# Kernel optimization log

Measured on AMD Instinct MI355X. Metric: run time of the kernel, lower is better.

## Reference

```python
import jax, jax.numpy as jnp
import numpy as np

D_MODEL = 512
NUM_HEADS = 8
D_K = D_MODEL // NUM_HEADS
SCALE = 1.0 / np.sqrt(D_K).astype(np.float32)


def _relative_shift(x):
    # x: (B, H, S, P) pos scores from Q @ P^T; Transformer-XL shift trick.
    b, h, s, p = x.shape
    x = jnp.pad(x, ((0, 0), (0, 0), (0, 0), (1, 0)))   # (B,H,S,P+1)
    x = x.reshape(b, h, p + 1, s)[:, :, 1:, :]          # drop first row
    x = x.reshape(b, h, s, p)[:, :, :, :s]
    return x


def setup_inputs() -> dict:
    key = jax.random.key(0)
    ks = jax.random.split(key, 10)
    B, S = 4, 2048
    glorot = lambda k: jax.random.uniform(
        k, (D_MODEL, D_MODEL), jnp.float32,
        -np.sqrt(6.0 / (2 * D_MODEL)), np.sqrt(6.0 / (2 * D_MODEL)))
    return {
        "inputs": jax.random.normal(ks[0], (B, S, D_MODEL), jnp.float32),
        "pos_enc": jax.random.normal(ks[1], (1, S, D_MODEL), jnp.float32),
        "W_q": glorot(ks[2]),
        "W_k": glorot(ks[3]),
        "W_v": glorot(ks[4]),
        "W_o": glorot(ks[5]),
        "W_pos": glorot(ks[6]),
        "u_bias": jnp.zeros((NUM_HEADS, D_K), jnp.float32),
        "v_bias": jnp.zeros((NUM_HEADS, D_K), jnp.float32),
    }


def reference(inputs, pos_enc, W_q, W_k, W_v, W_o, W_pos, u_bias, v_bias):
    B, S, _ = inputs.shape
    split = lambda x, b: x.reshape(b, S, NUM_HEADS, D_K).transpose(0, 2, 1, 3)
    Q = split(inputs @ W_q, B)        # (B,H,S,dk)
    K = split(inputs @ W_k, B)
    V = split(inputs @ W_v, B)
    P = split(pos_enc @ W_pos, 1)      # (1,H,S,dk)
    u = u_bias[None, :, None, :]
    v = v_bias[None, :, None, :]
    content_score = jnp.einsum('bhid,bhjd->bhij', Q + u, K)
    pos_score = jnp.einsum('bhid,xhjd->bhij', Q + v, P)  # broadcast over batch
    pos_score = _relative_shift(pos_score)
    scores = (content_score + pos_score) * SCALE
    attn = jax.nn.softmax(scores, axis=-1)  # no dropout (inference)
    context = jnp.einsum('bhij,bhjd->bhid', attn, V)
    context = context.transpose(0, 2, 1, 3).reshape(B, S, D_MODEL)
    return context @ W_o
```

## Files before the change

kernel.cpp:

```cpp
#include <hip/hip_runtime.h>
#include <hip/hip_bf16.h>
#include <math.h>

#define SEQ 2048
#define NH 8
#define DK 64
#define DM 512
#define QSCALE 0.18033688011112042f
#define PPAD (SEQ + 128)
#define POFF 64
#define KSTR 72
#define PSTR 36
#define ASTR 34

typedef unsigned short ushortT;
typedef short s16x8 __attribute__((ext_vector_type(8)));
typedef float f32x4 __attribute__((ext_vector_type(4)));

#define MFMA16 __builtin_amdgcn_mfma_f32_16x16x32_bf16

static __device__ __forceinline__ ushortT f2bf(float x) {
  __hip_bfloat16 h = __float2bfloat16(x);
  ushortT u;
  __builtin_memcpy(&u, &h, 2);
  return u;
}

static __device__ __forceinline__ float fexp2(float x) {
  return __builtin_amdgcn_exp2f(x);
}

static __device__ __forceinline__ s16x8 pack8(const float* p) {
  ushortT u[8];
#pragma unroll
  for (int i = 0; i < 8; ++i) u[i] = f2bf(p[i]);
  s16x8 out;
  __builtin_memcpy(&out, u, 16);
  return out;
}

static __device__ __forceinline__ int pinv(int j) {
  return (j < 16) ? ((j >> 2) * 8 + (j & 3)) : (((j >> 2) - 4) * 8 + 4 + (j & 3));
}

__global__ __launch_bounds__(256)
void cast_in(const float* __restrict__ X, const float* __restrict__ PE,
             ushortT* __restrict__ Xb, ushortT* __restrict__ PEb) {
  const size_t i4 = (size_t)blockIdx.x * 256 + threadIdx.x;
  const size_t NX = (size_t)4 * SEQ * DM / 4;
  const float4 v = (i4 < NX) ? *(const float4*)(X + i4 * 4)
                             : *(const float4*)(PE + (i4 - NX) * 4);
  ushortT o[4] = {f2bf(v.x), f2bf(v.y), f2bf(v.z), f2bf(v.w)};
  ushortT* dst = (i4 < NX) ? (Xb + i4 * 4) : (PEb + (i4 - NX) * 4);
  *(ulonglong1*)dst = *(ulonglong1*)o;
}

__global__ __launch_bounds__(256)
void transpose_w(const float* __restrict__ w0, const float* __restrict__ w1,
                 const float* __restrict__ w2, const float* __restrict__ w3,
                 const float* __restrict__ w4, ushortT* __restrict__ out) {
  __shared__ float ts[32][33];
  const int z = blockIdx.z;
  const float* w = (z == 0) ? w0 : (z == 1) ? w1 : (z == 2) ? w2 : (z == 3) ? w3 : w4;
  ushortT* o = out + (size_t)z * DM * DM;
  const int k0 = blockIdx.x * 32, n0 = blockIdx.y * 32;
  const int tx = threadIdx.x, ty = threadIdx.y;
#pragma unroll
  for (int i = 0; i < 4; ++i)
    ts[ty + i * 8][tx] = w[(size_t)(k0 + ty + i * 8) * DM + n0 + tx];
  __syncthreads();
#pragma unroll
  for (int i = 0; i < 4; ++i)
    o[(size_t)(n0 + ty + i * 8) * DM + k0 + tx] = f2bf(ts[tx][ty + i * 8]);
}

__global__ __launch_bounds__(256)
void gemm_mfma(const ushortT* __restrict__ A, const ushortT* __restrict__ Bt,
               const float* __restrict__ ubv, const float* __restrict__ vbv,
               ushortT* __restrict__ qu, ushortT* __restrict__ qv,
               ushortT* __restrict__ kb, ushortT* __restrict__ vt,
               float* __restrict__ of, int mode) {
  __shared__ ushortT As[128][ASTR];
  __shared__ ushortT Bs[128][ASTR];
  const int tid = threadIdx.x;
  const int w = tid >> 6, lane = tid & 63;
  const int c = lane & 15, q = lane >> 4;
  const int wm = w >> 1, wn = w & 1;
  const int m0 = blockIdx.x * 128, n0 = blockIdx.y * 128;
  const int lr = tid >> 1, lh = (tid & 1) * 16;

  f32x4 acc[4][4];
#pragma unroll
  for (int mt = 0; mt < 4; ++mt)
#pragma unroll
    for (int nt = 0; nt < 4; ++nt) acc[mt][nt] = (f32x4){0.f, 0.f, 0.f, 0.f};

  const ushortT* Ar = A + (size_t)(m0 + lr) * DM + lh;
  const ushortT* Br = Bt + (size_t)(n0 + lr) * DM + lh;
  uint4 a0 = *(const uint4*)(Ar);
  uint4 a1 = *(const uint4*)(Ar + 8);
  uint4 b0 = *(const uint4*)(Br);
  uint4 b1 = *(const uint4*)(Br + 8);

  for (int k0 = 0; k0 < DM; k0 += 32) {
    __syncthreads();
    *(uint4*)&As[lr][lh] = a0; *(uint4*)&As[lr][lh + 8] = a1;
    *(uint4*)&Bs[lr][lh] = b0; *(uint4*)&Bs[lr][lh + 8] = b1;
    __syncthreads();
    if (k0 + 32 < DM) {
      a0 = *(const uint4*)(Ar + k0 + 32);
      a1 = *(const uint4*)(Ar + k0 + 40);
      b0 = *(const uint4*)(Br + k0 + 32);
      b1 = *(const uint4*)(Br + k0 + 40);
    }
    s16x8 af[4], bf[4];
#pragma unroll
    for (int mt = 0; mt < 4; ++mt)
      af[mt] = *(const s16x8*)&As[wm * 64 + mt * 16 + c][q * 8];
#pragma unroll
    for (int nt = 0; nt < 4; ++nt)
      bf[nt] = *(const s16x8*)&Bs[wn * 64 + nt * 16 + c][q * 8];
#pragma unroll
    for (int mt = 0; mt < 4; ++mt)
#pragma unroll
      for (int nt = 0; nt < 4; ++nt)
        acc[mt][nt] = MFMA16(af[mt], bf[nt], acc[mt][nt], 0, 0, 0);
  }

#pragma unroll
  for (int mt = 0; mt < 4; ++mt)
#pragma unroll
    for (int nt = 0; nt < 4; ++nt)
#pragma unroll
      for (int r = 0; r < 4; ++r) {
        const int gm = m0 + wm * 64 + mt * 16 + q * 4 + r;
        const int gn = n0 + wn * 64 + nt * 16 + c;
        const float v = acc[mt][nt][r];
        const int bb = gm >> 11, s = gm & (SEQ - 1);
        if (mode == 0) {
          const int z = gn >> 9, gn5 = gn & 511;
          const int h = gn5 >> 6, d = gn5 & 63;
          if (z == 0) {
            const size_t base = (((size_t)bb * NH + h) * SEQ + s) * DK + d;
            qu[base] = f2bf((v + ubv[gn5]) * QSCALE);
            qv[base] = f2bf((v + vbv[gn5]) * QSCALE);
          } else if (z == 1) {
            kb[(((size_t)bb * NH + h) * SEQ + s) * DK + d] = f2bf(v);
          } else {
            const int s_il = (s & ~31) | pinv(s & 31);
            vt[(((size_t)bb * NH + h) * DK + d) * SEQ + s_il] = f2bf(v);
          }
        } else if (mode == 3) {
          const int h = gn >> 6, d = gn & 63;
          qu[((size_t)h * PPAD + POFF + gm) * DK + d] = f2bf(v);
        } else {
          of[(size_t)gm * DM + gn] = v;
        }
      }
}

static __device__ __forceinline__ f32x4 band_gemm(const ushortT* pb, int tile,
                                                  int c, int q, s16x8 a0, s16x8 a1) {
  const ushortT* pc = pb + (ptrdiff_t)(tile * 16 + c) * DK + q * 8;
  f32x4 G = {0.f, 0.f, 0.f, 0.f};
  G = MFMA16(a0, *(const s16x8*)pc, G, 0, 0, 0);
  G = MFMA16(a1, *(const s16x8*)(pc + 32), G, 0, 0, 0);
  return G;
}

__global__ __launch_bounds__(256, 3)
void attn_mfma(const ushortT* __restrict__ Qu, const ushortT* __restrict__ Qv,
               const ushortT* __restrict__ Kb, const ushortT* __restrict__ Vt,
               const ushortT* __restrict__ Pp, ushortT* __restrict__ ctxb) {
  const int n = blockIdx.x;
  const int xcd = n & 7, idx = n >> 3;
  const int b = idx >> 5, iblk = idx & 31;
  const int h = xcd, bh = b * 8 + h;
  const int tid = threadIdx.x;
  const int w = tid >> 6, lane = tid & 63;
  const int c = lane & 15, q = lane >> 4;
  const int i0 = iblk * 64;
  const int iw = i0 + w * 16;

  __shared__ ushortT Ks[64][KSTR];
  __shared__ ushortT Vs[64][KSTR];
  __shared__ float E1[4][16][PSTR];
  __shared__ float E2[4][16][PSTR];
  __shared__ float Lb[4][16];

  const ushortT* Qub = Qu + ((size_t)bh * SEQ + iw) * DK;
  const ushortT* Qvb = Qv + ((size_t)bh * SEQ + iw) * DK;
  const ushortT* Kbh = Kb + (size_t)bh * SEQ * DK;
  const ushortT* Vbh = Vt + (size_t)bh * DK * SEQ;
  const ushortT* Ph  = Pp + ((size_t)h * PPAD + POFF) * DK;

  const s16x8 qu0 = *(const s16x8*)(Qub + (size_t)c * DK + q * 8);
  const s16x8 qu1 = *(const s16x8*)(Qub + (size_t)c * DK + 32 + q * 8);
  s16x8 qv0 = *(const s16x8*)(Qvb + (size_t)c * DK + q * 8);
  s16x8 qv1 = *(const s16x8*)(Qvb + (size_t)c * DK + 32 + q * 8);

  int joff[8];
#pragma unroll
  for (int jj = 0; jj < 8; ++jj)
    joff[jj] = (jj < 4) ? (4 * q + jj) : (16 + 4 * q + (jj - 4));

  f32x4 O[4];
#pragma unroll
  for (int r = 0; r < 4; ++r) O[r] = (f32x4){0.f, 0.f, 0.f, 0.f};
  float lrow = 0.f;
  f32x4 e[3];
  bool hv1 = false, hv2 = false;
  const int jt = iw & ~31;
  const int m_w = q * 4;

  {
    const ushortT* gk = Kbh;
    uint4 k0v = *(const uint4*)(gk + tid * 8);
    uint4 k1v = *(const uint4*)(gk + 2048 + tid * 8);
    const ushortT* gv = Vbh + (size_t)(tid >> 2) * SEQ + (tid & 3) * 16;
    uint4 v0v = *(const uint4*)gv;
    uint4 v1v = *(const uint4*)(gv + 8);
    *(uint4*)&Ks[tid >> 3][(tid & 7) * 8] = k0v;
    *(uint4*)&Ks[32 + (tid >> 3)][(tid & 7) * 8] = k1v;
    *(uint4*)&Vs[tid >> 2][(tid & 3) * 16] = v0v;
    *(uint4*)&Vs[tid >> 2][(tid & 3) * 16 + 8] = v1v;
  }
  __syncthreads();

#define WRITE_BAND(ARR, ev)                                                   \
  _Pragma("unroll")                                                           \
  for (int t = 0; t < 3; ++t)                                                 \
    _Pragma("unroll")                                                         \
    for (int r = 0; r < 4; ++r) {                                             \
      const int kcol = t * 16 + c + (m_w + r) - 15;                           \
      if (kcol >= 0 && kcol < 32) ARR[w][m_w + r][pinv(kcol)] = (ev)[t][r];   \
    }

#define PV_FROM(pr, jl)                                                       \
  {                                                                           \
    lrow += pr[0] + pr[1] + pr[2] + pr[3] + pr[4] + pr[5] + pr[6] + pr[7];    \
    const s16x8 pa = pack8(pr);                                               \
    _Pragma("unroll")                                                         \
    for (int dt = 0; dt < 4; ++dt) {                                          \
      const s16x8 vb = *(const s16x8*)&Vs[dt * 16 + c][(jl) + q * 8];         \
      O[dt] = MFMA16(pa, vb, O[dt], 0, 0, 0);                                 \
    }                                                                         \
  }

  for (int ch = 0; ch < 32; ++ch) {
    const bool more = (ch + 1) < 32;
    uint4 k0v, k1v, v0v, v1v;
    if (more) {
      const ushortT* gk = Kbh + (size_t)(ch + 1) * 64 * DK;
      k0v = *(const uint4*)(gk + tid * 8);
      k1v = *(const uint4*)(gk + 2048 + tid * 8);
      const ushortT* gv = Vbh + (size_t)(tid >> 2) * SEQ + (ch + 1) * 64 + (tid & 3) * 16;
      v0v = *(const uint4*)gv;
      v1v = *(const uint4*)(gv + 8);
    }
#pragma unroll
    for (int t = 0; t < 2; ++t) {
      const int j0 = ch * 64 + t * 32;
      const int jl = t * 32;
      const int drel = j0 - iw;
      f32x4 S0 = {0.f, 0.f, 0.f, 0.f}, S1 = {0.f, 0.f, 0.f, 0.f};
      {
        const ushortT* ka = &Ks[jl + c][q * 8];
        S0 = MFMA16(*(const s16x8*)ka, qu0, S0, 0, 0, 0);
        S0 = MFMA16(*(const s16x8*)(ka + 32), qu1, S0, 0, 0, 0);
        const ushortT* ka2 = &Ks[jl + 16 + c][q * 8];
        S1 = MFMA16(*(const s16x8*)ka2, qu0, S1, 0, 0, 0);
        S1 = MFMA16(*(const s16x8*)(ka2 + 32), qu1, S1, 0, 0, 0);
      }
      if (j0 < jt) {
        const ushortT* pb1 = Ph + (ptrdiff_t)(drel + SEQ - 16) * DK;
        if (hv1) e[0] = e[2];
        else { e[0] = band_gemm(pb1, 0, c, q, qv0, qv1); hv1 = true; }
        e[1] = band_gemm(pb1, 1, c, q, qv0, qv1);
        e[2] = band_gemm(pb1, 2, c, q, qv0, qv1);
        WRITE_BAND(E1, e)
        const float* e1r = &E1[w][c][q * 8];
        float4 fA = *(const float4*)e1r, fB = *(const float4*)(e1r + 4);
        float pr[8] = {fexp2(S0[0] + fA.x), fexp2(S0[1] + fA.y),
                       fexp2(S0[2] + fA.z), fexp2(S0[3] + fA.w),
                       fexp2(S1[0] + fB.x), fexp2(S1[1] + fB.y),
                       fexp2(S1[2] + fB.z), fexp2(S1[3] + fB.w)};
        PV_FROM(pr, jl)
      } else if (j0 < jt + 64) {
        {
          const ushortT* pb1 = Ph + (ptrdiff_t)(drel + SEQ - 16) * DK;
          f32x4 t1[3];
          t1[0] = band_gemm(pb1, 0, c, q, qv0, qv1);
          t1[1] = band_gemm(pb1, 1, c, q, qv0, qv1);
          t1[2] = band_gemm(pb1, 2, c, q, qv0, qv1);
          WRITE_BAND(E1, t1)
        }
        {
          const s16x8 qw0 = *(const s16x8*)(Qvb + (size_t)(c + 1) * DK + q * 8);
          const s16x8 qw1 = *(const s16x8*)(Qvb + (size_t)(c + 1) * DK + 32 + q * 8);
          const ushortT* pb2 = Ph + (ptrdiff_t)(drel - 17) * DK;
          f32x4 t2[3];
          t2[0] = band_gemm(pb2, 0, c, q, qw0, qw1);
          t2[1] = band_gemm(pb2, 1, c, q, qw0, qw1);
          t2[2] = band_gemm(pb2, 2, c, q, qw0, qw1);
          WRITE_BAND(E2, t2)
        }
        const float* e1r = &E1[w][c][q * 8];
        const float* e2r = &E2[w][c][q * 8];
        float4 aA = *(const float4*)e1r, aB = *(const float4*)(e1r + 4);
        float4 bA = *(const float4*)e2r, bB = *(const float4*)(e2r + 4);
        float f1[8] = {aA.x, aA.y, aA.z, aA.w, aB.x, aB.y, aB.z, aB.w};
        float f2[8] = {bA.x, bA.y, bA.z, bA.w, bB.x, bB.y, bB.z, bB.w};
        float sv[8] = {S0[0], S0[1], S0[2], S0[3], S1[0], S1[1], S1[2], S1[3]};
        float pr[8];
#pragma unroll
        for (int jj = 0; jj < 8; ++jj) {
          const int dlt = drel + joff[jj] - c;
          const float g = (dlt <= 0) ? f1[jj] : ((dlt == 1) ? 0.0f : f2[jj]);
          pr[jj] = fexp2(sv[jj] + g);
        }
        PV_FROM(pr, jl)
      } else {
        if (!hv2) {
          qv0 = *(const s16x8*)(Qvb + (size_t)(c + 1) * DK + q * 8);
          qv1 = *(const s16x8*)(Qvb + (size_t)(c + 1) * DK + 32 + q * 8);
        }
        const ushortT* pb2 = Ph + (ptrdiff_t)(drel - 17) * DK;
        if (hv2) e[0] = e[2];
        else { e[0] = band_gemm(pb2, 0, c, q, qv0, qv1); hv2 = true; }
        e[1] = band_gemm(pb2, 1, c, q, qv0, qv1);
        e[2] = band_gemm(pb2, 2, c, q, qv0, qv1);
        WRITE_BAND(E1, e)
        const float* e1r = &E1[w][c][q * 8];
        float4 fA = *(const float4*)e1r, fB = *(const float4*)(e1r + 4);
        float pr[8] = {fexp2(S0[0] + fA.x), fexp2(S0[1] + fA.y),
                       fexp2(S0[2] + fA.z), fexp2(S0[3] + fA.w),
                       fexp2(S1[0] + fB.x), fexp2(S1[1] + fB.y),
                       fexp2(S1[2] + fB.z), fexp2(S1[3] + fB.w)};
        PV_FROM(pr, jl)
      }
    }
    __syncthreads();
    if (more) {
      *(uint4*)&Ks[tid >> 3][(tid & 7) * 8] = k0v;
      *(uint4*)&Ks[32 + (tid >> 3)][(tid & 7) * 8] = k1v;
      *(uint4*)&Vs[tid >> 2][(tid & 3) * 16] = v0v;
      *(uint4*)&Vs[tid >> 2][(tid & 3) * 16 + 8] = v1v;
    }
    __syncthreads();
  }

  lrow += __shfl_xor(lrow, 16);
  lrow += __shfl_xor(lrow, 32);
  if (q == 0) Lb[w][c] = lrow;
  float inv[4];
#pragma unroll
  for (int r = 0; r < 4; ++r) inv[r] = 1.0f / Lb[w][q * 4 + r];
#pragma unroll
  for (int dt = 0; dt < 4; ++dt)
#pragma unroll
    for (int r = 0; r < 4; ++r) {
      const int i = iw + q * 4 + r;
      ctxb[((size_t)b * SEQ + i) * DM + h * DK + dt * 16 + c] = f2bf(O[dt][r] * inv[r]);
    }
}

extern "C" void kernel_launch(void* const* d_in, const int* in_sizes, int n_in,
                              void* d_out, int out_size, void* d_ws, size_t ws_size,
                              hipStream_t stream) {
  (void)in_sizes; (void)n_in; (void)out_size; (void)ws_size;
  const float* X   = (const float*)d_in[0];
  const float* PE  = (const float*)d_in[1];
  const float* Wq  = (const float*)d_in[2];
  const float* Wk  = (const float*)d_in[3];
  const float* Wv  = (const float*)d_in[4];
  const float* Wo  = (const float*)d_in[5];
  const float* Wp  = (const float*)d_in[6];
  const float* ubv = (const float*)d_in[7];
  const float* vbv = (const float*)d_in[8];

  const size_t NX = (size_t)4 * SEQ * DM;
  const size_t NP = (size_t)SEQ * DM;
  const size_t NW = (size_t)DM * DM;
  ushortT* Xb  = (ushortT*)d_ws;
  ushortT* PEb = Xb + NX;
  ushortT* Wt  = PEb + NP;
  ushortT* qu  = Wt + 5 * NW;
  ushortT* qv  = qu + NX;
  ushortT* kb  = qv + NX;
  ushortT* vt  = kb + NX;
  ushortT* pp  = vt + NX;
  ushortT* ctx = pp + (size_t)NH * PPAD * DK;
  float* outp = (float*)d_out;

  hipLaunchKernelGGL(cast_in, dim3((NX + NP) / 4 / 256), dim3(256), 0, stream, X, PE, Xb, PEb);
  hipLaunchKernelGGL(transpose_w, dim3(16, 16, 5), dim3(32, 8), 0, stream, Wq, Wk, Wv, Wp, Wo, Wt);
  dim3 blk(256);
  hipLaunchKernelGGL(gemm_mfma, dim3(64, 12), blk, 0, stream, Xb, Wt, ubv, vbv,
                     qu, qv, kb, vt, (float*)nullptr, 0);
  hipLaunchKernelGGL(gemm_mfma, dim3(16, 4), blk, 0, stream, PEb, Wt + 3 * NW, ubv, vbv,
                     pp, (ushortT*)nullptr, (ushortT*)nullptr, (ushortT*)nullptr, (float*)nullptr, 3);
  hipLaunchKernelGGL(attn_mfma, dim3(1024), blk, 0, stream, qu, qv, kb, vt, pp, ctx);
  hipLaunchKernelGGL(gemm_mfma, dim3(64, 4), blk, 0, stream, ctx, Wt + 4 * NW, ubv, vbv,
                     (ushortT*)nullptr, (ushortT*)nullptr, (ushortT*)nullptr, (ushortT*)nullptr, outp, 4);
}
```

Measured before the change: 375.1 us.

## Use single-wave attention blocks loading K/V fragments directly from global memory

The attention kernel moves from 256-thread blocks that stage 64-key K/V chunks in shared memory, with two barriers per chunk, to 64-thread single-wave blocks (4096 of them). Each wave loads its K and V MFMA fragments straight from global memory for each 32-key step. The row-sum normalization now uses a wave shuffle instead of shared memory. This removes the barriers and the LDS staging, but K/V reuse across the four waves is lost, so global/L2 traffic rises about fourfold and load latency is no longer hidden by prefetching.

```diff
diff --git a/kernel.cpp b/kernel.cpp
--- a/kernel.cpp
+++ b/kernel.cpp
@@ -9,7 +9,6 @@
 #define QSCALE 0.18033688011112042f
 #define PPAD (SEQ + 128)
 #define POFF 64
-#define KSTR 72
 #define PSTR 36
 #define ASTR 34
 
@@ -168,25 +167,20 @@
   return G;
 }
 
-__global__ __launch_bounds__(256, 3)
+__global__ __launch_bounds__(64, 4)
 void attn_mfma(const ushortT* __restrict__ Qu, const ushortT* __restrict__ Qv,
                const ushortT* __restrict__ Kb, const ushortT* __restrict__ Vt,
                const ushortT* __restrict__ Pp, ushortT* __restrict__ ctxb) {
   const int n = blockIdx.x;
-  const int xcd = n & 7, idx = n >> 3;
-  const int b = idx >> 5, iblk = idx & 31;
-  const int h = xcd, bh = b * 8 + h;
-  const int tid = threadIdx.x;
-  const int w = tid >> 6, lane = tid & 63;
+  const int h = n & 7, idx = n >> 3;
+  const int b = idx >> 7;
+  const int iw = (idx & 127) * 16;
+  const int bh = b * 8 + h;
+  const int lane = threadIdx.x;
   const int c = lane & 15, q = lane >> 4;
-  const int i0 = iblk * 64;
-  const int iw = i0 + w * 16;
-
-  __shared__ ushortT Ks[64][KSTR];
-  __shared__ ushortT Vs[64][KSTR];
-  __shared__ float E1[4][16][PSTR];
-  __shared__ float E2[4][16][PSTR];
-  __shared__ float Lb[4][16];
+
+  __shared__ float E1[16][PSTR];
+  __shared__ float E2[16][PSTR];
 
   const ushortT* Qub = Qu + ((size_t)bh * SEQ + iw) * DK;
   const ushortT* Qvb = Qv + ((size_t)bh * SEQ + iw) * DK;
@@ -213,149 +207,117 @@
   const int jt = iw & ~31;
   const int m_w = q * 4;
 
-  {
-    const ushortT* gk = Kbh;
-    uint4 k0v = *(const uint4*)(gk + tid * 8);
-    uint4 k1v = *(const uint4*)(gk + 2048 + tid * 8);
-    const ushortT* gv = Vbh + (size_t)(tid >> 2) * SEQ + (tid & 3) * 16;
-    uint4 v0v = *(const uint4*)gv;
-    uint4 v1v = *(const uint4*)(gv + 8);
-    *(uint4*)&Ks[tid >> 3][(tid & 7) * 8] = k0v;
-    *(uint4*)&Ks[32 + (tid >> 3)][(tid & 7) * 8] = k1v;
-    *(uint4*)&Vs[tid >> 2][(tid & 3) * 16] = v0v;
-    *(uint4*)&Vs[tid >> 2][(tid & 3) * 16 + 8] = v1v;
-  }
-  __syncthreads();
-
 #define WRITE_BAND(ARR, ev)                                                   \
   _Pragma("unroll")                                                           \
   for (int t = 0; t < 3; ++t)                                                 \
     _Pragma("unroll")                                                         \
     for (int r = 0; r < 4; ++r) {                                             \
       const int kcol = t * 16 + c + (m_w + r) - 15;                           \
-      if (kcol >= 0 && kcol < 32) ARR[w][m_w + r][pinv(kcol)] = (ev)[t][r];   \
+      if (kcol >= 0 && kcol < 32) ARR[m_w + r][pinv(kcol)] = (ev)[t][r];      \
     }
 
-#define PV_FROM(pr, jl)                                                       \
+#define PV_FROM(pr)                                                           \
   {                                                                           \
     lrow += pr[0] + pr[1] + pr[2] + pr[3] + pr[4] + pr[5] + pr[6] + pr[7];    \
     const s16x8 pa = pack8(pr);                                               \
     _Pragma("unroll")                                                         \
-    for (int dt = 0; dt < 4; ++dt) {                                          \
-      const s16x8 vb = *(const s16x8*)&Vs[dt * 16 + c][(jl) + q * 8];         \
-      O[dt] = MFMA16(pa, vb, O[dt], 0, 0, 0);                                 \
-    }                                                                         \
+    for (int dt = 0; dt < 4; ++dt)                                            \
+      O[dt] = MFMA16(pa, vb[dt], O[dt], 0, 0, 0);                             \
   }
 
-  for (int ch = 0; ch < 32; ++ch) {
-    const bool more = (ch + 1) < 32;
-    uint4 k0v, k1v, v0v, v1v;
-    if (more) {
-      const ushortT* gk = Kbh + (size_t)(ch + 1) * 64 * DK;
-      k0v = *(const uint4*)(gk + tid * 8);
-      k1v = *(const uint4*)(gk + 2048 + tid * 8);
-      const ushortT* gv = Vbh + (size_t)(tid >> 2) * SEQ + (ch + 1) * 64 + (tid & 3) * 16;
-      v0v = *(const uint4*)gv;
-      v1v = *(const uint4*)(gv + 8);
+  for (int jb = 0; jb < 64; ++jb) {
+    const int j0 = jb * 32;
+    const int drel = j0 - iw;
+
+    const s16x8 kf0 = *(const s16x8*)(Kbh + (size_t)(j0 + c) * DK + q * 8);
+    const s16x8 kf1 = *(const s16x8*)(Kbh + (size_t)(j0 + c) * DK + 32 + q * 8);
+    const s16x8 kf2 = *(const s16x8*)(Kbh + (size_t)(j0 + 16 + c) * DK + q * 8);
+    const s16x8 kf3 = *(const s16x8*)(Kbh + (size_t)(j0 + 16 + c) * DK + 32 + q * 8);
+    s16x8 vb[4];
+#pragma unroll
+    for (int dt = 0; dt < 4; ++dt)
+      vb[dt] = *(const s16x8*)(Vbh + (size_t)(dt * 16 + c) * SEQ + j0 + q * 8);
+
+    f32x4 S0 = {0.f, 0.f, 0.f, 0.f}, S1 = {0.f, 0.f, 0.f, 0.f};
+    S0 = MFMA16(kf0, qu0, S0, 0, 0, 0);
+    S0 = MFMA16(kf1, qu1, S0, 0, 0, 0);
+    S1 = MFMA16(kf2, qu0, S1, 0, 0, 0);
+    S1 = MFMA16(kf3, qu1, S1, 0, 0, 0);
+
+    if (j0 < jt) {
+      const ushortT* pb1 = Ph + (ptrdiff_t)(drel + SEQ - 16) * DK;
+      if (hv1) e[0] = e[2];
+      else { e[0] = band_gemm(pb1, 0, c, q, qv0, qv1); hv1 = true; }
+      e[1] = band_gemm(pb1, 1, c, q, qv0, qv1);
+      e[2] = band_gemm(pb1, 2, c, q, qv0, qv1);
+      WRITE_BAND(E1, e)
+      const float* e1r = &E1[c][q * 8];
+      float4 fA = *(const float4*)e1r, fB = *(const float4*)(e1r + 4);
+      float pr[8] = {fexp2(S0[0] + fA.x), fexp2(S0[1] + fA.y),
+                     fexp2(S0[2] + fA.z), fexp2(S0[3] + fA.w),
+                     fexp2(S1[0] + fB.x), fexp2(S1[1] + fB.y),
+                     fexp2(S1[2] + fB.z), fexp2(S1[3] + fB.w)};
+      PV_FROM(pr)
+    } else if (j0 < jt + 64) {
+      {
+        const ushortT* pb1 = Ph + (ptrdiff_t)(drel + SEQ - 16) * DK;
+        f32x4 t1[3];
+        t1[0] = band_gemm(pb1, 0, c, q, qv0, qv1);
+        t1[1] = band_gemm(pb1, 1, c, q, qv0, qv1);
+        t1[2] = band_gemm(pb1, 2, c, q, qv0, qv1);
+        WRITE_BAND(E1, t1)
+      }
+      {
+        const s16x8 qw0 = *(const s16x8*)(Qvb + (size_t)(c + 1) * DK + q * 8);
+        const s16x8 qw1 = *(const s16x8*)(Qvb + (size_t)(c + 1) * DK + 32 + q * 8);
+        const ushortT* pb2 = Ph + (ptrdiff_t)(drel - 17) * DK;
+        f32x4 t2[3];
+        t2[0] = band_gemm(pb2, 0, c, q, qw0, qw1);
+        t2[1] = band_gemm(pb2, 1, c, q, qw0, qw1);
+        t2[2] = band_gemm(pb2, 2, c, q, qw0, qw1);
+        WRITE_BAND(E2, t2)
+      }
+      const float* e1r = &E1[c][q * 8];
+      const float* e2r = &E2[c][q * 8];
+      float4 aA = *(const float4*)e1r, aB = *(const float4*)(e1r + 4);
+      float4 bA = *(const float4*)e2r, bB = *(const float4*)(e2r + 4);
+      float f1[8] = {aA.x, aA.y, aA.z, aA.w, aB.x, aB.y, aB.z, aB.w};
+      float f2[8] = {bA.x, bA.y, bA.z, bA.w, bB.x, bB.y, bB.z, bB.w};
+      float sv[8] = {S0[0], S0[1], S0[2], S0[3], S1[0], S1[1], S1[2], S1[3]};
+      float pr[8];
+#pragma unroll
+      for (int jj = 0; jj < 8; ++jj) {
+        const int dlt = drel + joff[jj] - c;
+        const float g = (dlt <= 0) ? f1[jj] : ((dlt == 1) ? 0.0f : f2[jj]);
+        pr[jj] = fexp2(sv[jj] + g);
+      }
+      PV_FROM(pr)
+    } else {
+      if (!hv2) {
+        qv0 = *(const s16x8*)(Qvb + (size_t)(c + 1) * DK + q * 8);
+        qv1 = *(const s16x8*)(Qvb + (size_t)(c + 1) * DK + 32 + q * 8);
+      }
+      const ushortT* pb2 = Ph + (ptrdiff_t)(drel - 17) * DK;
+      if (hv2) e[0] = e[2];
+      else { e[0] = band_gemm(pb2, 0, c, q, qv0, qv1); hv2 = true; }
+      e[1] = band_gemm(pb2, 1, c, q, qv0, qv1);
+      e[2] = band_gemm(pb2, 2, c, q, qv0, qv1);
+      WRITE_BAND(E1, e)
+      const float* e1r = &E1[c][q * 8];
+      float4 fA = *(const float4*)e1r, fB = *(const float4*)(e1r + 4);
+      float pr[8] = {fexp2(S0[0] + fA.x), fexp2(S0[1] + fA.y),
+                     fexp2(S0[2] + fA.z), fexp2(S0[3] + fA.w),
+                     fexp2(S1[0] + fB.x), fexp2(S1[1] + fB.y),
+                     fexp2(S1[2] + fB.z), fexp2(S1[3] + fB.w)};
+      PV_FROM(pr)
     }
-#pragma unroll
-    for (int t = 0; t < 2; ++t) {
-      const int j0 = ch * 64 + t * 32;
-      const int jl = t * 32;
-      const int drel = j0 - iw;
-      f32x4 S0 = {0.f, 0.f, 0.f, 0.f}, S1 = {0.f, 0.f, 0.f, 0.f};
-      {
-        const ushortT* ka = &Ks[jl + c][q * 8];
-        S0 = MFMA16(*(const s16x8*)ka, qu0, S0, 0, 0, 0);
-        S0 = MFMA16(*(const s16x8*)(ka + 32), qu1, S0, 0, 0, 0);
-        const ushortT* ka2 = &Ks[jl + 16 + c][q * 8];
-        S1 = MFMA16(*(const s16x8*)ka2, qu0, S1, 0, 0, 0);
-        S1 = MFMA16(*(const s16x8*)(ka2 + 32), qu1, S1, 0, 0, 0);
-      }
-      if (j0 < jt) {
-        const ushortT* pb1 = Ph + (ptrdiff_t)(drel + SEQ - 16) * DK;
-        if (hv1) e[0] = e[2];
-        else { e[0] = band_gemm(pb1, 0, c, q, qv0, qv1); hv1 = true; }
-        e[1] = band_gemm(pb1, 1, c, q, qv0, qv1);
-        e[2] = band_gemm(pb1, 2, c, q, qv0, qv1);
-        WRITE_BAND(E1, e)
-        const float* e1r = &E1[w][c][q * 8];
-        float4 fA = *(const float4*)e1r, fB = *(const float4*)(e1r + 4);
-        float pr[8] = {fexp2(S0[0] + fA.x), fexp2(S0[1] + fA.y),
-                       fexp2(S0[2] + fA.z), fexp2(S0[3] + fA.w),
-                       fexp2(S1[0] + fB.x), fexp2(S1[1] + fB.y),
-                       fexp2(S1[2] + fB.z), fexp2(S1[3] + fB.w)};
-        PV_FROM(pr, jl)
-      } else if (j0 < jt + 64) {
-        {
-          const ushortT* pb1 = Ph + (ptrdiff_t)(drel + SEQ - 16) * DK;
-          f32x4 t1[3];
-          t1[0] = band_gemm(pb1, 0, c, q, qv0, qv1);
-          t1[1] = band_gemm(pb1, 1, c, q, qv0, qv1);
-          t1[2] = band_gemm(pb1, 2, c, q, qv0, qv1);
-          WRITE_BAND(E1, t1)
-        }
-        {
-          const s16x8 qw0 = *(const s16x8*)(Qvb + (size_t)(c + 1) * DK + q * 8);
-          const s16x8 qw1 = *(const s16x8*)(Qvb + (size_t)(c + 1) * DK + 32 + q * 8);
-          const ushortT* pb2 = Ph + (ptrdiff_t)(drel - 17) * DK;
-          f32x4 t2[3];
-          t2[0] = band_gemm(pb2, 0, c, q, qw0, qw1);
-          t2[1] = band_gemm(pb2, 1, c, q, qw0, qw1);
-          t2[2] = band_gemm(pb2, 2, c, q, qw0, qw1);
-          WRITE_BAND(E2, t2)
-        }
-        const float* e1r = &E1[w][c][q * 8];
-        const float* e2r = &E2[w][c][q * 8];
-        float4 aA = *(const float4*)e1r, aB = *(const float4*)(e1r + 4);
-        float4 bA = *(const float4*)e2r, bB = *(const float4*)(e2r + 4);
-        float f1[8] = {aA.x, aA.y, aA.z, aA.w, aB.x, aB.y, aB.z, aB.w};
-        float f2[8] = {bA.x, bA.y, bA.z, bA.w, bB.x, bB.y, bB.z, bB.w};
-        float sv[8] = {S0[0], S0[1], S0[2], S0[3], S1[0], S1[1], S1[2], S1[3]};
-        float pr[8];
-#pragma unroll
-        for (int jj = 0; jj < 8; ++jj) {
-          const int dlt = drel + joff[jj] - c;
-          const float g = (dlt <= 0) ? f1[jj] : ((dlt == 1) ? 0.0f : f2[jj]);
-          pr[jj] = fexp2(sv[jj] + g);
-        }
-        PV_FROM(pr, jl)
-      } else {
-        if (!hv2) {
-          qv0 = *(const s16x8*)(Qvb + (size_t)(c + 1) * DK + q * 8);
-          qv1 = *(const s16x8*)(Qvb + (size_t)(c + 1) * DK + 32 + q * 8);
-        }
-        const ushortT* pb2 = Ph + (ptrdiff_t)(drel - 17) * DK;
-        if (hv2) e[0] = e[2];
-        else { e[0] = band_gemm(pb2, 0, c, q, qv0, qv1); hv2 = true; }
-        e[1] = band_gemm(pb2, 1, c, q, qv0, qv1);
-        e[2] = band_gemm(pb2, 2, c, q, qv0, qv1);
-        WRITE_BAND(E1, e)
-        const float* e1r = &E1[w][c][q * 8];
-        float4 fA = *(const float4*)e1r, fB = *(const float4*)(e1r + 4);
-        float pr[8] = {fexp2(S0[0] + fA.x), fexp2(S0[1] + fA.y),
-                       fexp2(S0[2] + fA.z), fexp2(S0[3] + fA.w),
-                       fexp2(S1[0] + fB.x), fexp2(S1[1] + fB.y),
-                       fexp2(S1[2] + fB.z), fexp2(S1[3] + fB.w)};
-        PV_FROM(pr, jl)
-      }
-    }
-    __syncthreads();
-    if (more) {
-      *(uint4*)&Ks[tid >> 3][(tid & 7) * 8] = k0v;
-      *(uint4*)&Ks[32 + (tid >> 3)][(tid & 7) * 8] = k1v;
-      *(uint4*)&Vs[tid >> 2][(tid & 3) * 16] = v0v;
-      *(uint4*)&Vs[tid >> 2][(tid & 3) * 16 + 8] = v1v;
-    }
-    __syncthreads();
   }
 
   lrow += __shfl_xor(lrow, 16);
   lrow += __shfl_xor(lrow, 32);
-  if (q == 0) Lb[w][c] = lrow;
   float inv[4];
 #pragma unroll
-  for (int r = 0; r < 4; ++r) inv[r] = 1.0f / Lb[w][q * 4 + r];
+  for (int r = 0; r < 4; ++r) inv[r] = 1.0f / __shfl(lrow, m_w + r);
 #pragma unroll
   for (int dt = 0; dt < 4; ++dt)
 #pragma unroll
@@ -400,7 +362,7 @@
                      qu, qv, kb, vt, (float*)nullptr, 0);
   hipLaunchKernelGGL(gemm_mfma, dim3(16, 4), blk, 0, stream, PEb, Wt + 3 * NW, ubv, vbv,
                      pp, (ushortT*)nullptr, (ushortT*)nullptr, (ushortT*)nullptr, (float*)nullptr, 3);
-  hipLaunchKernelGGL(attn_mfma, dim3(1024), blk, 0, stream, qu, qv, kb, vt, pp, ctx);
+  hipLaunchKernelGGL(attn_mfma, dim3(4096), dim3(64), 0, stream, qu, qv, kb, vt, pp, ctx);
   hipLaunchKernelGGL(gemm_mfma, dim3(64, 4), blk, 0, stream, ctx, Wt + 4 * NW, ubv, vbv,
                      (ushortT*)nullptr, (ushortT*)nullptr, (ushortT*)nullptr, (ushortT*)nullptr, outp, 4);
 }
```

Measured after the change: 527.9 us. +40.7%, slower.

## Software-pipeline positional band GEMM one tile ahead with double-buffered LDS

Applied to the files above, without the earlier changes.

Computes the relative-position band scores for the next 32-column tile after the current tile's softmax and PV work, storing them in a double-buffered E1 LDS array. The aim is to hide the latency of the band MFMAs, the global P loads and the LDS write/read round trip behind independent work. The shifted Qv rows (qw) are now loaded once up front. This raises LDS use and register pressure, which could lower occupancy at the 3-blocks-per-SM launch bound.

```diff
diff --git a/kernel.cpp b/kernel.cpp
--- a/kernel.cpp
+++ b/kernel.cpp
@@ -168,6 +168,18 @@
   return G;
 }
 
+static __device__ __forceinline__ void write_band(float (*E)[PSTR], int c, int m_w,
+                                                  f32x4 b0, f32x4 b1, f32x4 b2) {
+  const f32x4 bb[3] = {b0, b1, b2};
+#pragma unroll
+  for (int t = 0; t < 3; ++t)
+#pragma unroll
+    for (int r = 0; r < 4; ++r) {
+      const int kcol = t * 16 + c + (m_w + r) - 15;
+      if (kcol >= 0 && kcol < 32) E[m_w + r][pinv(kcol)] = bb[t][r];
+    }
+}
+
 __global__ __launch_bounds__(256, 3)
 void attn_mfma(const ushortT* __restrict__ Qu, const ushortT* __restrict__ Qv,
                const ushortT* __restrict__ Kb, const ushortT* __restrict__ Vt,
@@ -184,7 +196,7 @@
 
   __shared__ ushortT Ks[64][KSTR];
   __shared__ ushortT Vs[64][KSTR];
-  __shared__ float E1[4][16][PSTR];
+  __shared__ float E1[4][2][16][PSTR];
   __shared__ float E2[4][16][PSTR];
   __shared__ float Lb[4][16];
 
@@ -196,8 +208,10 @@
 
   const s16x8 qu0 = *(const s16x8*)(Qub + (size_t)c * DK + q * 8);
   const s16x8 qu1 = *(const s16x8*)(Qub + (size_t)c * DK + 32 + q * 8);
-  s16x8 qv0 = *(const s16x8*)(Qvb + (size_t)c * DK + q * 8);
-  s16x8 qv1 = *(const s16x8*)(Qvb + (size_t)c * DK + 32 + q * 8);
+  const s16x8 qv0 = *(const s16x8*)(Qvb + (size_t)c * DK + q * 8);
+  const s16x8 qv1 = *(const s16x8*)(Qvb + (size_t)c * DK + 32 + q * 8);
+  const s16x8 qw0 = *(const s16x8*)(Qvb + (size_t)(c + 1) * DK + q * 8);
+  const s16x8 qw1 = *(const s16x8*)(Qvb + (size_t)(c + 1) * DK + 32 + q * 8);
 
   int joff[8];
 #pragma unroll
@@ -208,7 +222,7 @@
 #pragma unroll
   for (int r = 0; r < 4; ++r) O[r] = (f32x4){0.f, 0.f, 0.f, 0.f};
   float lrow = 0.f;
-  f32x4 e[3];
+  f32x4 e2c = (f32x4){0.f, 0.f, 0.f, 0.f};
   bool hv1 = false, hv2 = false;
   const int jt = iw & ~31;
   const int m_w = q * 4;
@@ -227,14 +241,14 @@
   }
   __syncthreads();
 
-#define WRITE_BAND(ARR, ev)                                                   \
-  _Pragma("unroll")                                                           \
-  for (int t = 0; t < 3; ++t)                                                 \
-    _Pragma("unroll")                                                         \
-    for (int r = 0; r < 4; ++r) {                                             \
-      const int kcol = t * 16 + c + (m_w + r) - 15;                           \
-      if (kcol >= 0 && kcol < 32) ARR[w][m_w + r][pinv(kcol)] = (ev)[t][r];   \
-    }
+  if (jt > 0) {
+    const ushortT* pb1 = Ph + (ptrdiff_t)(0 - iw + SEQ - 16) * DK;
+    f32x4 b0 = band_gemm(pb1, 0, c, q, qv0, qv1);
+    f32x4 b1 = band_gemm(pb1, 1, c, q, qv0, qv1);
+    e2c = band_gemm(pb1, 2, c, q, qv0, qv1);
+    hv1 = true;
+    write_band(E1[w][0], c, m_w, b0, b1, e2c);
+  }
 
 #define PV_FROM(pr, jl)                                                       \
   {                                                                           \
@@ -260,9 +274,12 @@
     }
 #pragma unroll
     for (int t = 0; t < 2; ++t) {
-      const int j0 = ch * 64 + t * 32;
+      const int nn = ch * 2 + t;
+      const int j0 = nn * 32;
       const int jl = t * 32;
       const int drel = j0 - iw;
+      const bool curB = (j0 >= jt) && (j0 < jt + 64);
+
       f32x4 S0 = {0.f, 0.f, 0.f, 0.f}, S1 = {0.f, 0.f, 0.f, 0.f};
       {
         const ushortT* ka = &Ks[jl + c][q * 8];
@@ -272,40 +289,23 @@
         S1 = MFMA16(*(const s16x8*)ka2, qu0, S1, 0, 0, 0);
         S1 = MFMA16(*(const s16x8*)(ka2 + 32), qu1, S1, 0, 0, 0);
       }
-      if (j0 < jt) {
-        const ushortT* pb1 = Ph + (ptrdiff_t)(drel + SEQ - 16) * DK;
-        if (hv1) e[0] = e[2];
-        else { e[0] = band_gemm(pb1, 0, c, q, qv0, qv1); hv1 = true; }
-        e[1] = band_gemm(pb1, 1, c, q, qv0, qv1);
-        e[2] = band_gemm(pb1, 2, c, q, qv0, qv1);
-        WRITE_BAND(E1, e)
-        const float* e1r = &E1[w][c][q * 8];
-        float4 fA = *(const float4*)e1r, fB = *(const float4*)(e1r + 4);
-        float pr[8] = {fexp2(S0[0] + fA.x), fexp2(S0[1] + fA.y),
-                       fexp2(S0[2] + fA.z), fexp2(S0[3] + fA.w),
-                       fexp2(S1[0] + fB.x), fexp2(S1[1] + fB.y),
-                       fexp2(S1[2] + fB.z), fexp2(S1[3] + fB.w)};
-        PV_FROM(pr, jl)
-      } else if (j0 < jt + 64) {
+
+      if (curB) {
         {
           const ushortT* pb1 = Ph + (ptrdiff_t)(drel + SEQ - 16) * DK;
-          f32x4 t1[3];
-          t1[0] = band_gemm(pb1, 0, c, q, qv0, qv1);
-          t1[1] = band_gemm(pb1, 1, c, q, qv0, qv1);
-          t1[2] = band_gemm(pb1, 2, c, q, qv0, qv1);
-          WRITE_BAND(E1, t1)
+          f32x4 b0 = band_gemm(pb1, 0, c, q, qv0, qv1);
+          f32x4 b1 = band_gemm(pb1, 1, c, q, qv0, qv1);
+          f32x4 b2 = band_gemm(pb1, 2, c, q, qv0, qv1);
+          write_band(E1[w][nn & 1], c, m_w, b0, b1, b2);
         }
         {
-          const s16x8 qw0 = *(const s16x8*)(Qvb + (size_t)(c + 1) * DK + q * 8);
-          const s16x8 qw1 = *(const s16x8*)(Qvb + (size_t)(c + 1) * DK + 32 + q * 8);
           const ushortT* pb2 = Ph + (ptrdiff_t)(drel - 17) * DK;
-          f32x4 t2[3];
-          t2[0] = band_gemm(pb2, 0, c, q, qw0, qw1);
-          t2[1] = band_gemm(pb2, 1, c, q, qw0, qw1);
-          t2[2] = band_gemm(pb2, 2, c, q, qw0, qw1);
-          WRITE_BAND(E2, t2)
+          f32x4 b0 = band_gemm(pb2, 0, c, q, qw0, qw1);
+          f32x4 b1 = band_gemm(pb2, 1, c, q, qw0, qw1);
+          f32x4 b2 = band_gemm(pb2, 2, c, q, qw0, qw1);
+          write_band(E2[w], c, m_w, b0, b1, b2);
         }
-        const float* e1r = &E1[w][c][q * 8];
+        const float* e1r = &E1[w][nn & 1][c][q * 8];
         const float* e2r = &E2[w][c][q * 8];
         float4 aA = *(const float4*)e1r, aB = *(const float4*)(e1r + 4);
         float4 bA = *(const float4*)e2r, bB = *(const float4*)(e2r + 4);
@@ -321,23 +321,38 @@
         }
         PV_FROM(pr, jl)
       } else {
-        if (!hv2) {
-          qv0 = *(const s16x8*)(Qvb + (size_t)(c + 1) * DK + q * 8);
-          qv1 = *(const s16x8*)(Qvb + (size_t)(c + 1) * DK + 32 + q * 8);
-        }
-        const ushortT* pb2 = Ph + (ptrdiff_t)(drel - 17) * DK;
-        if (hv2) e[0] = e[2];
-        else { e[0] = band_gemm(pb2, 0, c, q, qv0, qv1); hv2 = true; }
-        e[1] = band_gemm(pb2, 1, c, q, qv0, qv1);
-        e[2] = band_gemm(pb2, 2, c, q, qv0, qv1);
-        WRITE_BAND(E1, e)
-        const float* e1r = &E1[w][c][q * 8];
+        const float* e1r = &E1[w][nn & 1][c][q * 8];
         float4 fA = *(const float4*)e1r, fB = *(const float4*)(e1r + 4);
         float pr[8] = {fexp2(S0[0] + fA.x), fexp2(S0[1] + fA.y),
                        fexp2(S0[2] + fA.z), fexp2(S0[3] + fA.w),
                        fexp2(S1[0] + fB.x), fexp2(S1[1] + fB.y),
                        fexp2(S1[2] + fB.z), fexp2(S1[3] + fB.w)};
         PV_FROM(pr, jl)
+      }
+
+      if (nn + 1 < 64) {
+        const int j0n = j0 + 32;
+        const bool nxtB = (j0n >= jt) && (j0n < jt + 64);
+        if (!nxtB) {
+          const int dreln = j0n - iw;
+          if (j0n < jt) {
+            const ushortT* pb1 = Ph + (ptrdiff_t)(dreln + SEQ - 16) * DK;
+            f32x4 b0;
+            if (hv1) b0 = e2c;
+            else { b0 = band_gemm(pb1, 0, c, q, qv0, qv1); hv1 = true; }
+            f32x4 b1 = band_gemm(pb1, 1, c, q, qv0, qv1);
+            e2c = band_gemm(pb1, 2, c, q, qv0, qv1);
+            write_band(E1[w][(nn + 1) & 1], c, m_w, b0, b1, e2c);
+          } else {
+            const ushortT* pb2 = Ph + (ptrdiff_t)(dreln - 17) * DK;
+            f32x4 b0;
+            if (hv2) b0 = e2c;
+            else { b0 = band_gemm(pb2, 0, c, q, qw0, qw1); hv2 = true; }
+            f32x4 b1 = band_gemm(pb2, 1, c, q, qw0, qw1);
+            e2c = band_gemm(pb2, 2, c, q, qw0, qw1);
+            write_band(E1[w][(nn + 1) & 1], c, m_w, b0, b1, e2c);
+          }
+        }
       }
     }
     __syncthreads();
```

New measurement: 358.6 us (median of 3 runs). 4.4% less time.
